# Optimization experiments

Hardware: AMD Instinct MI355X
Metric: run time of the kernel (lower is better)

The kernel has to match this reference:

```python
import jax, jax.numpy as jnp
import numpy as np

EPS = 1e-5


def setup_inputs() -> dict:
    key = jax.random.key(0)
    k1, k2 = jax.random.split(key)
    N, F = 65536, 1024
    return {
        "real": jax.random.normal(k1, (N, F), dtype=jnp.float32),
        "imag": jax.random.normal(k2, (N, F), dtype=jnp.float32),
        "gamma_rr": jnp.ones((F,), dtype=jnp.float32),
        "gamma_ri": jnp.zeros((F,), dtype=jnp.float32),
        "gamma_ii": jnp.ones((F,), dtype=jnp.float32),
        "beta_real": jnp.zeros((F,), dtype=jnp.float32),
        "beta_imag": jnp.zeros((F,), dtype=jnp.float32),
    }


def reference(real, imag, gamma_rr, gamma_ri, gamma_ii, beta_real, beta_imag):
    # Training-mode path: batch statistics over dim 0.
    mean_r = real.mean(axis=0)
    mean_i = imag.mean(axis=0)
    cr = real - mean_r          # [N, F]
    ci = imag - mean_i
    # Per-feature 2x2 covariance (eps added on diagonal, as in the torch code).
    C_rr = (cr * cr).mean(axis=0) + EPS
    C_ii = (ci * ci).mean(axis=0) + EPS
    C_ri = (cr * ci).mean(axis=0)
    # Closed-form inverse matrix square root of the SPD 2x2 covariance.
    # For M SPD 2x2: s = sqrt(det M), t = sqrt(tr M + 2 s),
    #   M^{-1/2} = [[C_ii + s, -C_ri], [-C_ri, C_rr + s]] / (s * t).
    # Equivalent to eigh-based whitening; eigvals >= EPS so the torch
    # clamp_min(eps) is a no-op.
    s = jnp.sqrt(C_rr * C_ii - C_ri * C_ri)
    t = jnp.sqrt(C_rr + C_ii + 2.0 * s)
    denom = s * t
    W_rr = (C_ii + s) / denom
    W_ii = (C_rr + s) / denom
    W_ri = -C_ri / denom
    # Whiten (W is symmetric 2x2 per feature, broadcast over batch).
    white_r = W_rr * cr + W_ri * ci
    white_i = W_ri * cr + W_ii * ci
    # Affine transform with symmetric Gamma and complex bias beta.
    out_r = gamma_rr * white_r + gamma_ri * white_i + beta_real
    out_i = gamma_ri * white_r + gamma_ii * white_i + beta_imag
    return out_r, out_i
```

## Files before the change

kernel.cpp:

```cpp
#include <hip/hip_runtime.h>

#define FEAT 1024
#define EPS 1e-5f


__global__ __launch_bounds__(256) void stats_kernel(const float* __restrict__ real,
                                                    const float* __restrict__ imag,
                                                    float* __restrict__ ws,
                                                    int nrows) {
    const int f4 = threadIdx.x * 4;
    float sr[4]  = {0.f, 0.f, 0.f, 0.f};
    float si[4]  = {0.f, 0.f, 0.f, 0.f};
    float srr[4] = {0.f, 0.f, 0.f, 0.f};
    float sii[4] = {0.f, 0.f, 0.f, 0.f};
    float sri[4] = {0.f, 0.f, 0.f, 0.f};

    for (int row = blockIdx.x; row < nrows; row += gridDim.x) {
        const size_t off = (size_t)row * FEAT + f4;
        const float4 r  = *(const float4*)(real + off);
        const float4 im = *(const float4*)(imag + off);
        const float rv[4]  = {r.x, r.y, r.z, r.w};
        const float iv[4]  = {im.x, im.y, im.z, im.w};
#pragma unroll
        for (int k = 0; k < 4; ++k) {
            sr[k]  += rv[k];
            si[k]  += iv[k];
            srr[k] = fmaf(rv[k], rv[k], srr[k]);
            sii[k] = fmaf(iv[k], iv[k], sii[k]);
            sri[k] = fmaf(rv[k], iv[k], sri[k]);
        }
    }

#pragma unroll
    for (int k = 0; k < 4; ++k) {
        atomicAdd(&ws[0 * FEAT + f4 + k], sr[k]);
        atomicAdd(&ws[1 * FEAT + f4 + k], si[k]);
        atomicAdd(&ws[2 * FEAT + f4 + k], srr[k]);
        atomicAdd(&ws[3 * FEAT + f4 + k], sii[k]);
        atomicAdd(&ws[4 * FEAT + f4 + k], sri[k]);
    }
}

__global__ __launch_bounds__(256) void finalize_kernel(const float* __restrict__ g_rr_p,
                                                       const float* __restrict__ g_ri_p,
                                                       const float* __restrict__ g_ii_p,
                                                       const float* __restrict__ b_r_p,
                                                       const float* __restrict__ b_i_p,
                                                       float* __restrict__ ws,
                                                       float inv_n) {
    const int f = blockIdx.x * blockDim.x + threadIdx.x;
    if (f >= FEAT) return;

    const float mr = ws[0 * FEAT + f] * inv_n;
    const float mi = ws[1 * FEAT + f] * inv_n;
    const float Crr = ws[2 * FEAT + f] * inv_n - mr * mr + EPS;
    const float Cii = ws[3 * FEAT + f] * inv_n - mi * mi + EPS;
    const float Cri = ws[4 * FEAT + f] * inv_n - mr * mi;

    const float s  = sqrtf(Crr * Cii - Cri * Cri);
    const float tt = sqrtf(Crr + Cii + 2.0f * s);
    const float inv_denom = 1.0f / (s * tt);
    const float Wrr = (Cii + s) * inv_denom;
    const float Wii = (Crr + s) * inv_denom;
    const float Wri = -Cri * inv_denom;

    const float grr = g_rr_p[f], gri = g_ri_p[f], gii = g_ii_p[f];
    const float Arr = grr * Wrr + gri * Wri;
    const float Ari = grr * Wri + gri * Wii;
    const float Air = gri * Wrr + gii * Wri;
    const float Aii = gri * Wri + gii * Wii;
    const float Br  = b_r_p[f] - Arr * mr - Ari * mi;
    const float Bi  = b_i_p[f] - Air * mr - Aii * mi;

    ws[5 * FEAT + f]  = Arr;
    ws[6 * FEAT + f]  = Ari;
    ws[7 * FEAT + f]  = Air;
    ws[8 * FEAT + f]  = Aii;
    ws[9 * FEAT + f]  = Br;
    ws[10 * FEAT + f] = Bi;
}

__global__ __launch_bounds__(256) void apply_kernel(const float* __restrict__ real,
                                                    const float* __restrict__ imag,
                                                    const float* __restrict__ ws,
                                                    float* __restrict__ out,
                                                    int nrows) {
    const int f4 = threadIdx.x * 4;
    const float4 Arr = *(const float4*)(ws + 5 * FEAT + f4);
    const float4 Ari = *(const float4*)(ws + 6 * FEAT + f4);
    const float4 Air = *(const float4*)(ws + 7 * FEAT + f4);
    const float4 Aii = *(const float4*)(ws + 8 * FEAT + f4);
    const float4 Br  = *(const float4*)(ws + 9 * FEAT + f4);
    const float4 Bi  = *(const float4*)(ws + 10 * FEAT + f4);

    float* __restrict__ out_i = out + (size_t)nrows * FEAT;

    for (int row = blockIdx.x; row < nrows; row += gridDim.x) {
        const size_t off = (size_t)row * FEAT + f4;
        const float4 r  = *(const float4*)(real + off);
        const float4 im = *(const float4*)(imag + off);

        float4 o_r, o_i;
        o_r.x = fmaf(Arr.x, r.x, fmaf(Ari.x, im.x, Br.x));
        o_r.y = fmaf(Arr.y, r.y, fmaf(Ari.y, im.y, Br.y));
        o_r.z = fmaf(Arr.z, r.z, fmaf(Ari.z, im.z, Br.z));
        o_r.w = fmaf(Arr.w, r.w, fmaf(Ari.w, im.w, Br.w));
        o_i.x = fmaf(Air.x, r.x, fmaf(Aii.x, im.x, Bi.x));
        o_i.y = fmaf(Air.y, r.y, fmaf(Aii.y, im.y, Bi.y));
        o_i.z = fmaf(Air.z, r.z, fmaf(Aii.z, im.z, Bi.z));
        o_i.w = fmaf(Air.w, r.w, fmaf(Aii.w, im.w, Bi.w));

        *(float4*)(out + off)   = o_r;
        *(float4*)(out_i + off) = o_i;
    }
}

extern "C" void kernel_launch(void* const* d_in, const int* in_sizes, int n_in,
                              void* d_out, int out_size, void* d_ws, size_t ws_size,
                              hipStream_t stream) {
    const float* real = (const float*)d_in[0];
    const float* imag = (const float*)d_in[1];
    const float* g_rr = (const float*)d_in[2];
    const float* g_ri = (const float*)d_in[3];
    const float* g_ii = (const float*)d_in[4];
    const float* b_r  = (const float*)d_in[5];
    const float* b_i  = (const float*)d_in[6];
    float* out = (float*)d_out;
    float* ws  = (float*)d_ws;

    const int nrows = in_sizes[0] / FEAT;

    hipMemsetAsync(ws, 0, 5 * FEAT * sizeof(float), stream);

    stats_kernel<<<1024, 256, 0, stream>>>(real, imag, ws, nrows);

    finalize_kernel<<<4, 256, 0, stream>>>(g_rr, g_ri, g_ii, b_r, b_i, ws,
                                           1.0f / (float)nrows);

    apply_kernel<<<2048, 256, 0, stream>>>(real, imag, ws, out, nrows);
}
```

Before: 1.032 ms.

## Unroll row loops, reverse apply order for cache reuse, add nontemporal stores

The stats kernel now handles four rows per iteration with all loads issued up front, and its grid doubles to 2048 blocks. The apply kernel handles row pairs, walks rows in reverse so the rows the stats pass read last (likely still in the last-level cache) are read first, and writes outputs with nontemporal stores so they do not evict input data. The aim is more memory-level parallelism and less DRAM traffic on this bandwidth-bound two-pass normalization. The new loops assume nrows is divisible by 4 and by 2, so any leftover rows would be skipped, and the extra atomics from the larger grid add a little contention.

Measured after the change: 1.049 ms. No clear change (+1.6%).

```diff
diff --git a/kernel.cpp b/kernel.cpp
--- a/kernel.cpp
+++ b/kernel.cpp
@@ -2,6 +2,8 @@
 
 #define FEAT 1024
 #define EPS 1e-5f
+
+typedef float f32x4 __attribute__((ext_vector_type(4)));
 
 
 __global__ __launch_bounds__(256) void stats_kernel(const float* __restrict__ real,
@@ -15,21 +17,33 @@
     float sii[4] = {0.f, 0.f, 0.f, 0.f};
     float sri[4] = {0.f, 0.f, 0.f, 0.f};
 
-    for (int row = blockIdx.x; row < nrows; row += gridDim.x) {
-        const size_t off = (size_t)row * FEAT + f4;
-        const float4 r  = *(const float4*)(real + off);
-        const float4 im = *(const float4*)(imag + off);
-        const float rv[4]  = {r.x, r.y, r.z, r.w};
-        const float iv[4]  = {im.x, im.y, im.z, im.w};
-#pragma unroll
-        for (int k = 0; k < 4; ++k) {
-            sr[k]  += rv[k];
-            si[k]  += iv[k];
-            srr[k] = fmaf(rv[k], rv[k], srr[k]);
-            sii[k] = fmaf(iv[k], iv[k], sii[k]);
-            sri[k] = fmaf(rv[k], iv[k], sri[k]);
-        }
+#define ACCUM(RV, IV)                               \
+    _Pragma("unroll")                               \
+    for (int k = 0; k < 4; ++k) {                   \
+        sr[k] += RV[k];                             \
+        si[k] += IV[k];                             \
+        srr[k] = fmaf(RV[k], RV[k], srr[k]);        \
+        sii[k] = fmaf(IV[k], IV[k], sii[k]);        \
+        sri[k] = fmaf(RV[k], IV[k], sri[k]);        \
     }
+
+    const int nchunks = nrows >> 2;
+    for (int c = blockIdx.x; c < nchunks; c += gridDim.x) {
+        const size_t base = ((size_t)c * 4) * FEAT + f4;
+        const f32x4 r0 = *(const f32x4*)(real + base);
+        const f32x4 i0 = *(const f32x4*)(imag + base);
+        const f32x4 r1 = *(const f32x4*)(real + base + FEAT);
+        const f32x4 i1 = *(const f32x4*)(imag + base + FEAT);
+        const f32x4 r2 = *(const f32x4*)(real + base + 2 * FEAT);
+        const f32x4 i2 = *(const f32x4*)(imag + base + 2 * FEAT);
+        const f32x4 r3 = *(const f32x4*)(real + base + 3 * FEAT);
+        const f32x4 i3 = *(const f32x4*)(imag + base + 3 * FEAT);
+        ACCUM(r0, i0)
+        ACCUM(r1, i1)
+        ACCUM(r2, i2)
+        ACCUM(r3, i3)
+    }
+#undef ACCUM
 
 #pragma unroll
     for (int k = 0; k < 4; ++k) {
@@ -86,32 +100,36 @@
                                                     float* __restrict__ out,
                                                     int nrows) {
     const int f4 = threadIdx.x * 4;
-    const float4 Arr = *(const float4*)(ws + 5 * FEAT + f4);
-    const float4 Ari = *(const float4*)(ws + 6 * FEAT + f4);
-    const float4 Air = *(const float4*)(ws + 7 * FEAT + f4);
-    const float4 Aii = *(const float4*)(ws + 8 * FEAT + f4);
-    const float4 Br  = *(const float4*)(ws + 9 * FEAT + f4);
-    const float4 Bi  = *(const float4*)(ws + 10 * FEAT + f4);
+    const f32x4 Arr = *(const f32x4*)(ws + 5 * FEAT + f4);
+    const f32x4 Ari = *(const f32x4*)(ws + 6 * FEAT + f4);
+    const f32x4 Air = *(const f32x4*)(ws + 7 * FEAT + f4);
+    const f32x4 Aii = *(const f32x4*)(ws + 8 * FEAT + f4);
+    const f32x4 Br  = *(const f32x4*)(ws + 9 * FEAT + f4);
+    const f32x4 Bi  = *(const f32x4*)(ws + 10 * FEAT + f4);
 
     float* __restrict__ out_i = out + (size_t)nrows * FEAT;
 
-    for (int row = blockIdx.x; row < nrows; row += gridDim.x) {
-        const size_t off = (size_t)row * FEAT + f4;
-        const float4 r  = *(const float4*)(real + off);
-        const float4 im = *(const float4*)(imag + off);
+    const int npairs = nrows >> 1;
+    for (int p = blockIdx.x; p < npairs; p += gridDim.x) {
+        const int pr = npairs - 1 - p;
+        const size_t base = ((size_t)pr * 2) * FEAT + f4;
+        const f32x4 r0 = *(const f32x4*)(real + base);
+        const f32x4 i0 = *(const f32x4*)(imag + base);
+        const f32x4 r1 = *(const f32x4*)(real + base + FEAT);
+        const f32x4 i1 = *(const f32x4*)(imag + base + FEAT);
 
-        float4 o_r, o_i;
-        o_r.x = fmaf(Arr.x, r.x, fmaf(Ari.x, im.x, Br.x));
-        o_r.y = fmaf(Arr.y, r.y, fmaf(Ari.y, im.y, Br.y));
-        o_r.z = fmaf(Arr.z, r.z, fmaf(Ari.z, im.z, Br.z));
-        o_r.w = fmaf(Arr.w, r.w, fmaf(Ari.w, im.w, Br.w));
-        o_i.x = fmaf(Air.x, r.x, fmaf(Aii.x, im.x, Bi.x));
-        o_i.y = fmaf(Air.y, r.y, fmaf(Aii.y, im.y, Bi.y));
-        o_i.z = fmaf(Air.z, r.z, fmaf(Aii.z, im.z, Bi.z));
-        o_i.w = fmaf(Air.w, r.w, fmaf(Aii.w, im.w, Bi.w));
-
-        *(float4*)(out + off)   = o_r;
-        *(float4*)(out_i + off) = o_i;
+        f32x4 or0, oi0, or1, oi1;
+#pragma unroll
+        for (int k = 0; k < 4; ++k) {
+            or0[k] = fmaf(Arr[k], r0[k], fmaf(Ari[k], i0[k], Br[k]));
+            oi0[k] = fmaf(Air[k], r0[k], fmaf(Aii[k], i0[k], Bi[k]));
+            or1[k] = fmaf(Arr[k], r1[k], fmaf(Ari[k], i1[k], Br[k]));
+            oi1[k] = fmaf(Air[k], r1[k], fmaf(Aii[k], i1[k], Bi[k]));
+        }
+        __builtin_nontemporal_store(or0, (f32x4*)(out + base));
+        __builtin_nontemporal_store(oi0, (f32x4*)(out_i + base));
+        __builtin_nontemporal_store(or1, (f32x4*)(out + base + FEAT));
+        __builtin_nontemporal_store(oi1, (f32x4*)(out_i + base + FEAT));
     }
 }
 
@@ -132,7 +150,7 @@
 
     hipMemsetAsync(ws, 0, 5 * FEAT * sizeof(float), stream);
 
-    stats_kernel<<<1024, 256, 0, stream>>>(real, imag, ws, nrows);
+    stats_kernel<<<2048, 256, 0, stream>>>(real, imag, ws, nrows);
 
     finalize_kernel<<<4, 256, 0, stream>>>(g_rr, g_ri, g_ii, b_r, b_i, ws,
                                            1.0f / (float)nrows);
```
